# Kernel tuning notes

Measured on AMD Instinct MI355X. Metric: run time of the kernel, lower is better.

## Reference

```python
import jax, jax.numpy as jnp
import numpy as np

B, T, D, K = 64, 1024, 256, 1024
DECAY = 0.99      # ema_decay
BETA = 0.25       # commitment_cost
EPS = 1e-5


def setup_inputs() -> dict:
    key = jax.random.key(0)
    k1, k2 = jax.random.split(key, 2)
    z = jax.random.normal(k1, (B, T, D), dtype=jnp.float32)
    # nn.init.uniform_(embedding.weight, -1/K, 1/K)
    embed = jax.random.uniform(k2, (K, D), dtype=jnp.float32,
                               minval=-1.0 / K, maxval=1.0 / K)
    ema_count = jnp.zeros((K,), dtype=jnp.float32)
    ema_weight = embed  # buffer initialized as a clone of the weight
    return {"z": z, "embed": embed, "ema_count": ema_count, "ema_weight": ema_weight}


def reference(z, embed, ema_count, ema_weight):
    Bq, Tq, Dq = z.shape
    zf = z.reshape(-1, Dq)  # [N, D], N = B*T
    # squared euclidean distances: [N, K]
    dist = (zf * zf).sum(axis=1, keepdims=True) \
        - 2.0 * (zf @ embed.T) \
        + (embed * embed).sum(axis=1)
    idx = jnp.argmin(dist, axis=1)                      # [N]
    q = embed[idx].reshape(Bq, Tq, Dq)                  # nearest codebook vectors

    commit = jnp.mean((z - jax.lax.stop_gradient(q)) ** 2)
    codebook = jnp.mean((q - jax.lax.stop_gradient(z)) ** 2)
    vq_loss = codebook + BETA * commit

    # straight-through estimator
    q_st = z + jax.lax.stop_gradient(q - z)

    # EMA codebook update (training-mode, no_grad in torch)
    counts = jax.ops.segment_sum(jnp.ones((zf.shape[0],), zf.dtype), idx, num_segments=K)
    dw = jax.ops.segment_sum(zf, idx, num_segments=K)   # one_hot.T @ z_flat, [K, D]
    new_count = DECAY * ema_count + (1.0 - DECAY) * counts
    new_ema_w = DECAY * ema_weight + (1.0 - DECAY) * dw
    n = new_count.sum()
    cs = (new_count + EPS) / (n + K * EPS) * n          # laplace-smoothed counts
    new_embed = new_ema_w / cs[:, None]

    return (q_st, vq_loss, idx.reshape(Bq, Tq), new_embed, new_count, new_ema_w)
```

## Files before the change

### kernel.cpp

```cpp
#include <hip/hip_runtime.h>
#include <cfloat>

#define N_Q     65536
#define D_DIM   256
#define K_CODES 1024
#define DELTA   0.004f
#define MARGIN  0.001f
#define SW_CAP  1536

#define OUT_QST   0
#define OUT_LOSS  16777216
#define OUT_IDX   16777217
#define OUT_EMBED 16842753
#define OUT_COUNT 17104897
#define OUT_EMAW  17105921

#define WS_IDX    0u
#define WS_ZZ     262144u
#define WS_PERM   524288u
#define WS_PACK   786432u
#define WS_EN     1310720u
#define WS_ICNT   1314816u
#define WS_OFFS   1318912u
#define WS_OFFW   1323008u
#define WS_CNTF   1327104u
#define WS_CS     1331200u
#define WS_ET     1335296u
#define WS_LOSSB  1859584u

typedef short          bf16x8 __attribute__((ext_vector_type(8)));
typedef unsigned short u16x8  __attribute__((ext_vector_type(8)));
typedef float          f32x4  __attribute__((ext_vector_type(4)));

__device__ inline unsigned short f2bf(float x) {
    unsigned u = __float_as_uint(x);
    u += 0x7FFFu + ((u >> 16) & 1u);
    return (unsigned short)(u >> 16);
}
__device__ inline float bf2f(unsigned short h) {
    return __uint_as_float((unsigned)h << 16);
}
__device__ inline u16x8 pack8(float4 a, float4 b) {
    u16x8 p;
    p[0]=f2bf(a.x); p[1]=f2bf(a.y); p[2]=f2bf(a.z); p[3]=f2bf(a.w);
    p[4]=f2bf(b.x); p[5]=f2bf(b.y); p[6]=f2bf(b.z); p[7]=f2bf(b.w);
    return p;
}
__device__ inline void gll16(const void* g, void* l) {
    __builtin_amdgcn_global_load_lds(
        (const __attribute__((address_space(1))) unsigned int*)g,
        (__attribute__((address_space(3))) unsigned int*)l, 16, 0, 0);
}

__global__ void rownorm2_kernel(const float* __restrict__ x, float* __restrict__ out)
{
    int wave = threadIdx.x >> 6, lane = threadIdx.x & 63;
    int row  = blockIdx.x * 4 + wave;
    const float4 v = *(const float4*)&x[(size_t)row * D_DIM + lane * 4];
    float s = v.x * v.x + v.y * v.y + v.z * v.z + v.w * v.w;
    #pragma unroll
    for (int m = 32; m >= 1; m >>= 1) s += __shfl_down(s, m, 64);
    if (lane == 0) out[row] = s;
}

__global__ void conv_e_kernel(const float* __restrict__ e,
                              unsigned short* __restrict__ et)
{
    int tid = blockIdx.x * 256 + threadIdx.x;
    int k16 = tid >> 9, d8 = (tid >> 4) & 31, col = tid & 15;
    const float* src = &e[(size_t)(k16 * 16 + col) * D_DIM + d8 * 8];
    float4 a = *(const float4*)&src[0];
    float4 b = *(const float4*)&src[4];
    *(u16x8*)&et[(size_t)tid * 8] = pack8(a, b);
}

__launch_bounds__(256, 2)
__global__ void sweep_kernel(const float* __restrict__ z,
                             const float* __restrict__ embed,
                             const unsigned short* __restrict__ et,
                             const float* __restrict__ enorm,
                             const float* __restrict__ zz,
                             unsigned long long* __restrict__ pack)
{
    __shared__ unsigned short Eb[2][16384];
    __shared__ unsigned list[SW_CAP];
    __shared__ unsigned short s1h[SW_CAP];
    __shared__ float Ens[K_CODES];
    __shared__ float rminS[128];
    __shared__ int lcnt;

    const int t = threadIdx.x;
    const int w = t >> 6, lane = t & 63;
    const int col = lane & 15, quad = lane >> 4;
    const int qbase = blockIdx.x * 128;

    if (t == 0) lcnt = 0;
    for (int i = t; i < K_CODES; i += 256) Ens[i] = enorm[i];

    {
        const unsigned short* src = et + w * 4096 + lane * 8;
        unsigned short* dst = &Eb[0][w * 4096];
        #pragma unroll
        for (int i = 0; i < 8; ++i) gll16(src + i * 512, dst + i * 512);
    }

    bf16x8 A[2][8];
    #pragma unroll
    for (int rt = 0; rt < 2; ++rt)
        #pragma unroll
        for (int ds = 0; ds < 8; ++ds) {
            const float* zp = &z[(size_t)(qbase + w*32 + rt*16 + col) * D_DIM
                                 + ds*32 + quad*8];
            float4 a = *(const float4*)zp;
            float4 b = *(const float4*)(zp + 4);
            u16x8 p = pack8(a, b);
            A[rt][ds] = *(bf16x8*)&p;
        }

    float rmin[2][4];
    #pragma unroll
    for (int rt = 0; rt < 2; ++rt)
        #pragma unroll
        for (int rg = 0; rg < 4; ++rg)
            rmin[rt][rg] = FLT_MAX;

    __syncthreads();

    #pragma unroll 1
    for (int kc = 0; kc < 16; ++kc) {
        if (kc < 15) {
            const unsigned short* src = et + (kc + 1) * 16384 + w * 4096 + lane * 8;
            unsigned short* dst = &Eb[(kc + 1) & 1][w * 4096];
            #pragma unroll
            for (int i = 0; i < 8; ++i) gll16(src + i * 512, dst + i * 512);
        }

        const unsigned short* buf = Eb[kc & 1];
        f32x4 acc[2][4];
        #pragma unroll
        for (int rt = 0; rt < 2; ++rt)
            #pragma unroll
            for (int ct = 0; ct < 4; ++ct)
                acc[rt][ct] = (f32x4){0.f, 0.f, 0.f, 0.f};

        #pragma unroll
        for (int ds = 0; ds < 8; ++ds) {
            bf16x8 B[4];
            #pragma unroll
            for (int ct = 0; ct < 4; ++ct)
                B[ct] = *(const bf16x8*)&buf[((ct*32 + ds*4 + quad)*16 + col)*8];
            #pragma unroll
            for (int ct = 0; ct < 4; ++ct) {
                acc[0][ct] = __builtin_amdgcn_mfma_f32_16x16x32_bf16(A[0][ds], B[ct], acc[0][ct], 0, 0, 0);
                acc[1][ct] = __builtin_amdgcn_mfma_f32_16x16x32_bf16(A[1][ds], B[ct], acc[1][ct], 0, 0, 0);
            }
        }

        float en[4];
        #pragma unroll
        for (int ct = 0; ct < 4; ++ct) en[ct] = Ens[kc*64 + ct*16 + col];

        #pragma unroll
        for (int rt = 0; rt < 2; ++rt) {
            #pragma unroll
            for (int rg = 0; rg < 4; ++rg) {
                float s1v[4];
                #pragma unroll
                for (int ct = 0; ct < 4; ++ct)
                    s1v[ct] = fmaf(-2.0f, acc[rt][ct][rg], en[ct]);
                float m = fminf(fminf(s1v[0], s1v[1]), fminf(s1v[2], s1v[3]));
                #pragma unroll
                for (int mm = 1; mm < 16; mm <<= 1)
                    m = fminf(m, __shfl_xor(m, mm, 64));
                rmin[rt][rg] = fminf(rmin[rt][rg], m);
                float thr = rmin[rt][rg] + DELTA;
                #pragma unroll
                for (int ct = 0; ct < 4; ++ct) {
                    if (s1v[ct] <= thr) {
                        int k    = kc*64 + ct*16 + col;
                        int qloc = w*32 + rt*16 + quad*4 + rg;
                        int pos  = atomicAdd(&lcnt, 1);
                        if (pos < SW_CAP) {
                            list[pos] = ((unsigned)qloc << 10) | (unsigned)k;
                            s1h[pos]  = f2bf(s1v[ct]);
                        } else {
                            int qg = qbase + qloc;
                            double dd = 0.0;
                            for (int d = 0; d < D_DIM; d += 4) {
                                float4 a = *(const float4*)&z[(size_t)qg*D_DIM + d];
                                float4 b = *(const float4*)&embed[(size_t)k*D_DIM + d];
                                dd += (double)a.x*b.x + (double)a.y*b.y
                                    + (double)a.z*b.z + (double)a.w*b.w;
                            }
                            float s = (zz[qg] - 2.0f*(float)dd) + en[ct];
                            unsigned long long pk =
                                ((unsigned long long)__float_as_uint(s) << 32) | (unsigned)k;
                            atomicMin(&pack[qg], pk);
                        }
                    }
                }
            }
        }

        __syncthreads();
    }

    if (col == 0) {
        #pragma unroll
        for (int rt = 0; rt < 2; ++rt)
            #pragma unroll
            for (int rg = 0; rg < 4; ++rg)
                rminS[w*32 + rt*16 + quad*4 + rg] = rmin[rt][rg];
    }
    __syncthreads();

    int cnt = min(lcnt, SW_CAP);
    int gid = t >> 3, gl = t & 7;
    for (int e = gid; e < cnt; e += 32) {
        unsigned ent = list[e];
        int qloc = (int)(ent >> 10), k = (int)(ent & 1023u);
        if (bf2f(s1h[e]) > rminS[qloc] + (DELTA + MARGIN)) continue;
        int qg = qbase + qloc;
        const float* zp  = &z[(size_t)qg * D_DIM + gl * 32];
        const float* epf = &embed[(size_t)k * D_DIM + gl * 32];
        double d0 = 0.0, d1 = 0.0;
        #pragma unroll
        for (int i = 0; i < 4; ++i) {
            float4 a  = *(const float4*)&zp[i*8];
            float4 b  = *(const float4*)&epf[i*8];
            float4 c  = *(const float4*)&zp[i*8 + 4];
            float4 dv = *(const float4*)&epf[i*8 + 4];
            d0 += (double)a.x*b.x + (double)a.y*b.y + (double)a.z*b.z + (double)a.w*b.w;
            d1 += (double)c.x*dv.x + (double)c.y*dv.y + (double)c.z*dv.z + (double)c.w*dv.w;
        }
        double dd = d0 + d1;
        #pragma unroll
        for (int m = 1; m < 8; m <<= 1) dd += __shfl_xor(dd, m, 64);
        if (gl == 0) {
            float s = (zz[qg] - 2.0f*(float)dd) + enorm[k];
            unsigned long long pk =
                ((unsigned long long)__float_as_uint(s) << 32) | (unsigned)k;
            atomicMin(&pack[qg], pk);
        }
    }
}

__global__ void unpack_kernel(const unsigned long long* __restrict__ pack,
                              int* __restrict__ idx_i,
                              float* __restrict__ idx_f,
                              int* __restrict__ icnt)
{
    int n = blockIdx.x * 256 + threadIdx.x;
    int k = (int)(pack[n] & 0xffffffffull);
    idx_i[n] = k;
    idx_f[n] = (float)k;
    atomicAdd(&icnt[k], 1);
}

__global__ void scan_kernel(const int* __restrict__ icnt,
                            int* __restrict__ offs,
                            int* __restrict__ offw,
                            float* __restrict__ cntf)
{
    __shared__ int s[1024];
    int t = threadIdx.x;
    int v0 = icnt[t];
    s[t] = v0;
    __syncthreads();
    for (int d = 1; d < 1024; d <<= 1) {
        int v = (t >= d) ? s[t - d] : 0;
        __syncthreads();
        s[t] += v;
        __syncthreads();
    }
    int excl = s[t] - v0;
    offs[t] = excl;
    offw[t] = excl;
    cntf[t] = (float)v0;
}

__global__ void fill_kernel(const int* __restrict__ idx,
                            int* __restrict__ offw,
                            int* __restrict__ perm)
{
    int n = blockIdx.x * 256 + threadIdx.x;
    int k = idx[n];
    int pos = atomicAdd(&offw[k], 1);
    perm[pos] = n;
}

__global__ void qst_loss_kernel(const float* __restrict__ z,
                                const float* __restrict__ embed,
                                const int* __restrict__ idx,
                                float* __restrict__ qst,
                                double* __restrict__ lossb)
{
    int tid = blockIdx.x * blockDim.x + threadIdx.x;
    int e0  = tid * 4;
    int n   = e0 >> 8, d = e0 & 255;
    int k   = idx[n];
    const float4 q4 = *(const float4*)&embed[(size_t)k * D_DIM + d];
    const float4 z4 = *(const float4*)&z[e0];
    float4 o;
    o.x = z4.x + (q4.x - z4.x);
    o.y = z4.y + (q4.y - z4.y);
    o.z = z4.z + (q4.z - z4.z);
    o.w = z4.w + (q4.w - z4.w);
    *(float4*)&qst[e0] = o;
    float dx = z4.x - q4.x, dy = z4.y - q4.y, dz = z4.z - q4.z, dw = z4.w - q4.w;
    float s = dx * dx + dy * dy + dz * dz + dw * dw;
    #pragma unroll
    for (int m = 32; m >= 1; m >>= 1) s += __shfl_down(s, m, 64);
    __shared__ float ps[4];
    int wave = threadIdx.x >> 6, lane = threadIdx.x & 63;
    if (lane == 0) ps[wave] = s;
    __syncthreads();
    if (threadIdx.x == 0)
        atomicAdd(&lossb[blockIdx.x & 1023],
                  (double)((ps[0] + ps[1]) + (ps[2] + ps[3])));
}

__global__ void fin_counts_kernel(const float* __restrict__ ema_count,
                                  const float* __restrict__ cntf,
                                  const double* __restrict__ lossb,
                                  float* __restrict__ out_count,
                                  float* __restrict__ out_loss,
                                  float* __restrict__ cs)
{
    __shared__ float  red[1024];
    __shared__ double dred[1024];
    int t = threadIdx.x;
    float c = 0.99f * ema_count[t] + 0.01f * cntf[t];
    out_count[t] = c;
    red[t]  = c;
    dred[t] = lossb[t];
    __syncthreads();
    for (int s = 512; s >= 1; s >>= 1) {
        if (t < s) { red[t] += red[t + s]; dred[t] += dred[t + s]; }
        __syncthreads();
    }
    float n = red[0];
    cs[t] = (c + 1e-5f) / (n + 1024.0f * 1e-5f) * n;
    if (t == 0) {
        float m = (float)(dred[0] / (double)((size_t)N_Q * D_DIM));
        out_loss[0] = m + 0.25f * m;
    }
}

__global__ void accum_embed_kernel(const float* __restrict__ z,
                                   const int* __restrict__ perm,
                                   const int* __restrict__ icnt,
                                   const int* __restrict__ offs,
                                   const float* __restrict__ cs,
                                   const float* __restrict__ ema_w,
                                   float* __restrict__ out_embed,
                                   float* __restrict__ out_emaw)
{
    __shared__ int rows[256];
    int k = blockIdx.x, t = threadIdx.x;
    int cnt = icnt[k], off = offs[k];
    double a0 = 0.0, a1 = 0.0, a2 = 0.0, a3 = 0.0;
    for (int base = 0; base < cnt; base += 256) {
        int m = min(256, cnt - base);
        __syncthreads();
        if (t < m) rows[t] = perm[off + base + t];
        __syncthreads();
        int r = 0;
        for (; r + 4 <= m; r += 4) {
            a0 += (double)z[(size_t)rows[r+0] * D_DIM + t];
            a1 += (double)z[(size_t)rows[r+1] * D_DIM + t];
            a2 += (double)z[(size_t)rows[r+2] * D_DIM + t];
            a3 += (double)z[(size_t)rows[r+3] * D_DIM + t];
        }
        for (; r < m; ++r) a0 += (double)z[(size_t)rows[r] * D_DIM + t];
    }
    double acc = (a0 + a1) + (a2 + a3);
    float w = 0.99f * ema_w[(size_t)k * D_DIM + t] + 0.01f * (float)acc;
    out_emaw[(size_t)k * D_DIM + t]  = w;
    out_embed[(size_t)k * D_DIM + t] = w / cs[k];
}

extern "C" void kernel_launch(void* const* d_in, const int* in_sizes, int n_in,
                              void* d_out, int out_size, void* d_ws, size_t ws_size,
                              hipStream_t stream)
{
    const float* z          = (const float*)d_in[0];
    const float* embed      = (const float*)d_in[1];
    const float* ema_count  = (const float*)d_in[2];
    const float* ema_weight = (const float*)d_in[3];
    float* out = (float*)d_out;
    char*  ws  = (char*)d_ws;

    int*      ws_idx  = (int*)(ws + WS_IDX);
    float*    ws_zz   = (float*)(ws + WS_ZZ);
    int*      ws_perm = (int*)(ws + WS_PERM);
    unsigned long long* ws_pack = (unsigned long long*)(ws + WS_PACK);
    float*    ws_en   = (float*)(ws + WS_EN);
    int*      ws_icnt = (int*)(ws + WS_ICNT);
    int*      ws_offs = (int*)(ws + WS_OFFS);
    int*      ws_offw = (int*)(ws + WS_OFFW);
    float*    ws_cntf = (float*)(ws + WS_CNTF);
    float*    ws_cs   = (float*)(ws + WS_CS);
    unsigned short* ws_et = (unsigned short*)(ws + WS_ET);
    double*   ws_lb   = (double*)(ws + WS_LOSSB);

    hipMemsetAsync(ws + WS_PACK,  0xFF, (size_t)N_Q * 8, stream);
    hipMemsetAsync(ws + WS_ICNT,  0, 4096, stream);
    hipMemsetAsync(ws + WS_LOSSB, 0, 8192, stream);

    rownorm2_kernel<<<K_CODES / 4, 256, 0, stream>>>(embed, ws_en);
    rownorm2_kernel<<<N_Q / 4,     256, 0, stream>>>(z, ws_zz);
    conv_e_kernel<<<128, 256, 0, stream>>>(embed, ws_et);

    sweep_kernel<<<N_Q / 128, 256, 0, stream>>>(z, embed, ws_et, ws_en, ws_zz,
                                                ws_pack);

    unpack_kernel<<<N_Q / 256, 256, 0, stream>>>(ws_pack, ws_idx,
                                                 out + OUT_IDX, ws_icnt);
    scan_kernel<<<1, 1024, 0, stream>>>(ws_icnt, ws_offs, ws_offw, ws_cntf);
    fill_kernel<<<N_Q / 256, 256, 0, stream>>>(ws_idx, ws_offw, ws_perm);
    qst_loss_kernel<<<(N_Q * (D_DIM / 4)) / 256, 256, 0, stream>>>(
        z, embed, ws_idx, out + OUT_QST, ws_lb);
    fin_counts_kernel<<<1, 1024, 0, stream>>>(ema_count, ws_cntf, ws_lb,
                                              out + OUT_COUNT, out + OUT_LOSS, ws_cs);
    accum_embed_kernel<<<K_CODES, 256, 0, stream>>>(z, ws_perm, ws_icnt, ws_offs,
                                                    ws_cs, ema_weight,
                                                    out + OUT_EMBED, out + OUT_EMAW);
}
```

Baseline: 332.2 us.

## Fuse prep kernels, compute z norms in sweep, defer overflow rescoring to spill kernel

Replaces the three memsets, the two rownorm launches and the embed conversion with a single prep kernel. The z row norms are now computed inside the sweep kernel from the values it already loads for the bf16 conversion. Candidate overflow past the shared list no longer runs a serial fp64 dot product inline; entries go to a global spill list that a separate kernel rescores. The per-row min reduction is batched across eight rows using ds_swizzle instead of shfl_xor. This trades fewer launches and less z traffic for an extra spill launch, and the spill buffer reuses the idx workspace region.

```diff
diff --git a/kernel.cpp b/kernel.cpp
--- a/kernel.cpp
+++ b/kernel.cpp
@@ -7,6 +7,7 @@
 #define DELTA   0.004f
 #define MARGIN  0.001f
 #define SW_CAP  1536
+#define SPILL_CAP 65536
 
 #define OUT_QST   0
 #define OUT_LOSS  16777216
@@ -27,6 +28,7 @@
 #define WS_CS     1331200u
 #define WS_ET     1335296u
 #define WS_LOSSB  1859584u
+#define WS_SPCNT  1867776u
 
 typedef short          bf16x8 __attribute__((ext_vector_type(8)));
 typedef unsigned short u16x8  __attribute__((ext_vector_type(8)));
@@ -51,27 +53,48 @@
         (const __attribute__((address_space(1))) unsigned int*)g,
         (__attribute__((address_space(3))) unsigned int*)l, 16, 0, 0);
 }
-
-__global__ void rownorm2_kernel(const float* __restrict__ x, float* __restrict__ out)
-{
-    int wave = threadIdx.x >> 6, lane = threadIdx.x & 63;
-    int row  = blockIdx.x * 4 + wave;
-    const float4 v = *(const float4*)&x[(size_t)row * D_DIM + lane * 4];
-    float s = v.x * v.x + v.y * v.y + v.z * v.z + v.w * v.w;
-    #pragma unroll
-    for (int m = 32; m >= 1; m >>= 1) s += __shfl_down(s, m, 64);
-    if (lane == 0) out[row] = s;
-}
-
-__global__ void conv_e_kernel(const float* __restrict__ e,
-                              unsigned short* __restrict__ et)
-{
-    int tid = blockIdx.x * 256 + threadIdx.x;
-    int k16 = tid >> 9, d8 = (tid >> 4) & 31, col = tid & 15;
-    const float* src = &e[(size_t)(k16 * 16 + col) * D_DIM + d8 * 8];
-    float4 a = *(const float4*)&src[0];
-    float4 b = *(const float4*)&src[4];
-    *(u16x8*)&et[(size_t)tid * 8] = pack8(a, b);
+#define SWZMIN(x, PAT) fminf((x), __int_as_float( \
+    __builtin_amdgcn_ds_swizzle(__float_as_int(x), (PAT))))
+
+__global__ void prep_kernel(const float* __restrict__ embed,
+                            unsigned short* __restrict__ et,
+                            unsigned long long* __restrict__ pack,
+                            float* __restrict__ enorm,
+                            int* __restrict__ icnt,
+                            double* __restrict__ lossb,
+                            int* __restrict__ spc)
+{
+    int b = blockIdx.x, t = threadIdx.x;
+    if (b < 128) {
+        int tid = b * 256 + t;
+        int k16 = tid >> 9, d8 = (tid >> 4) & 31, col = tid & 15;
+        const float* src = &embed[(size_t)(k16 * 16 + col) * D_DIM + d8 * 8];
+        float4 a = *(const float4*)&src[0];
+        float4 c = *(const float4*)&src[4];
+        *(u16x8*)&et[(size_t)tid * 8] = pack8(a, c);
+        unsigned long long* p = pack + (size_t)tid * 2;
+        p[0] = ~0ull; p[1] = ~0ull;
+    } else {
+        int b2 = b - 128;
+        int wave = t >> 6, lane = t & 63;
+        int rbase = (b2 * 4 + wave) * 8;
+        for (int i = 0; i < 8; ++i) {
+            int r = rbase + i;
+            const float4 v = *(const float4*)&embed[(size_t)r * D_DIM + lane * 4];
+            float s = v.x * v.x + v.y * v.y + v.z * v.z + v.w * v.w;
+            #pragma unroll
+            for (int m = 32; m >= 1; m >>= 1) s += __shfl_down(s, m, 64);
+            if (lane == 0) enorm[r] = s;
+        }
+        if (b2 == 0) {
+            #pragma unroll
+            for (int i = 0; i < 4; ++i) {
+                icnt[t * 4 + i] = 0;
+                lossb[t * 4 + i] = 0.0;
+            }
+            if (t == 0) *spc = 0;
+        }
+    }
 }
 
 __launch_bounds__(256, 2)
@@ -79,14 +102,17 @@
                              const float* __restrict__ embed,
                              const unsigned short* __restrict__ et,
                              const float* __restrict__ enorm,
-                             const float* __restrict__ zz,
-                             unsigned long long* __restrict__ pack)
+                             float* __restrict__ zzg,
+                             unsigned long long* __restrict__ pack,
+                             unsigned* __restrict__ spill,
+                             int* __restrict__ spc)
 {
     __shared__ unsigned short Eb[2][16384];
     __shared__ unsigned list[SW_CAP];
     __shared__ unsigned short s1h[SW_CAP];
     __shared__ float Ens[K_CODES];
     __shared__ float rminS[128];
+    __shared__ float zzS[128];
     __shared__ int lcnt;
 
     const int t = threadIdx.x;
@@ -106,23 +132,30 @@
 
     bf16x8 A[2][8];
     #pragma unroll
-    for (int rt = 0; rt < 2; ++rt)
+    for (int rt = 0; rt < 2; ++rt) {
+        float s = 0.f;
         #pragma unroll
         for (int ds = 0; ds < 8; ++ds) {
             const float* zp = &z[(size_t)(qbase + w*32 + rt*16 + col) * D_DIM
                                  + ds*32 + quad*8];
             float4 a = *(const float4*)zp;
             float4 b = *(const float4*)(zp + 4);
+            s += a.x*a.x + a.y*a.y + a.z*a.z + a.w*a.w
+               + b.x*b.x + b.y*b.y + b.z*b.z + b.w*b.w;
             u16x8 p = pack8(a, b);
             A[rt][ds] = *(bf16x8*)&p;
         }
-
-    float rmin[2][4];
+        s += __shfl_xor(s, 16, 64);
+        s += __shfl_xor(s, 32, 64);
+        if (quad == 0) {
+            zzg[qbase + w*32 + rt*16 + col] = s;
+            zzS[w*32 + rt*16 + col] = s;
+        }
+    }
+
+    float rmin[8];
     #pragma unroll
-    for (int rt = 0; rt < 2; ++rt)
-        #pragma unroll
-        for (int rg = 0; rg < 4; ++rg)
-            rmin[rt][rg] = FLT_MAX;
+    for (int i = 0; i < 8; ++i) rmin[i] = FLT_MAX;
 
     __syncthreads();
 
@@ -156,51 +189,66 @@
             }
         }
 
-        float en[4];
-        #pragma unroll
-        for (int ct = 0; ct < 4; ++ct) en[ct] = Ens[kc*64 + ct*16 + col];
-
-        #pragma unroll
-        for (int rt = 0; rt < 2; ++rt) {
+        float en4[4];
+        #pragma unroll
+        for (int ct = 0; ct < 4; ++ct) en4[ct] = Ens[kc*64 + ct*16 + col];
+
+        float s1v[2][4][4];
+        #pragma unroll
+        for (int rt = 0; rt < 2; ++rt)
+            #pragma unroll
+            for (int ct = 0; ct < 4; ++ct)
+                #pragma unroll
+                for (int rg = 0; rg < 4; ++rg)
+                    s1v[rt][ct][rg] = fmaf(-2.0f, acc[rt][ct][rg], en4[ct]);
+
+        float m8[8];
+        #pragma unroll
+        for (int rt = 0; rt < 2; ++rt)
+            #pragma unroll
+            for (int rg = 0; rg < 4; ++rg)
+                m8[rt*4+rg] = fminf(fminf(s1v[rt][0][rg], s1v[rt][1][rg]),
+                                    fminf(s1v[rt][2][rg], s1v[rt][3][rg]));
+
+        #pragma unroll
+        for (int i = 0; i < 8; ++i) m8[i] = SWZMIN(m8[i], 0x041F);
+        #pragma unroll
+        for (int i = 0; i < 8; ++i) m8[i] = SWZMIN(m8[i], 0x081F);
+        #pragma unroll
+        for (int i = 0; i < 8; ++i) m8[i] = SWZMIN(m8[i], 0x101F);
+        #pragma unroll
+        for (int i = 0; i < 8; ++i) m8[i] = SWZMIN(m8[i], 0x201F);
+
+        float thrv[8];
+        #pragma unroll
+        for (int i = 0; i < 8; ++i) {
+            rmin[i] = fminf(rmin[i], m8[i]);
+            thrv[i] = rmin[i] + DELTA;
+        }
+
+        #pragma unroll
+        for (int rt = 0; rt < 2; ++rt)
             #pragma unroll
             for (int rg = 0; rg < 4; ++rg) {
-                float s1v[4];
-                #pragma unroll
-                for (int ct = 0; ct < 4; ++ct)
-                    s1v[ct] = fmaf(-2.0f, acc[rt][ct][rg], en[ct]);
-                float m = fminf(fminf(s1v[0], s1v[1]), fminf(s1v[2], s1v[3]));
-                #pragma unroll
-                for (int mm = 1; mm < 16; mm <<= 1)
-                    m = fminf(m, __shfl_xor(m, mm, 64));
-                rmin[rt][rg] = fminf(rmin[rt][rg], m);
-                float thr = rmin[rt][rg] + DELTA;
+                float th = thrv[rt*4+rg];
                 #pragma unroll
                 for (int ct = 0; ct < 4; ++ct) {
-                    if (s1v[ct] <= thr) {
+                    if (s1v[rt][ct][rg] <= th) {
                         int k    = kc*64 + ct*16 + col;
                         int qloc = w*32 + rt*16 + quad*4 + rg;
                         int pos  = atomicAdd(&lcnt, 1);
                         if (pos < SW_CAP) {
                             list[pos] = ((unsigned)qloc << 10) | (unsigned)k;
-                            s1h[pos]  = f2bf(s1v[ct]);
+                            s1h[pos]  = f2bf(s1v[rt][ct][rg]);
                         } else {
-                            int qg = qbase + qloc;
-                            double dd = 0.0;
-                            for (int d = 0; d < D_DIM; d += 4) {
-                                float4 a = *(const float4*)&z[(size_t)qg*D_DIM + d];
-                                float4 b = *(const float4*)&embed[(size_t)k*D_DIM + d];
-                                dd += (double)a.x*b.x + (double)a.y*b.y
-                                    + (double)a.z*b.z + (double)a.w*b.w;
-                            }
-                            float s = (zz[qg] - 2.0f*(float)dd) + en[ct];
-                            unsigned long long pk =
-                                ((unsigned long long)__float_as_uint(s) << 32) | (unsigned)k;
-                            atomicMin(&pack[qg], pk);
+                            int sp = atomicAdd(spc, 1);
+                            if (sp < SPILL_CAP)
+                                spill[sp] = ((unsigned)(qbase + qloc) << 10)
+                                          | (unsigned)k;
                         }
                     }
                 }
             }
-        }
 
         __syncthreads();
     }
@@ -210,7 +258,7 @@
         for (int rt = 0; rt < 2; ++rt)
             #pragma unroll
             for (int rg = 0; rg < 4; ++rg)
-                rminS[w*32 + rt*16 + quad*4 + rg] = rmin[rt][rg];
+                rminS[w*32 + rt*16 + quad*4 + rg] = rmin[rt*4+rg];
     }
     __syncthreads();
 
@@ -234,6 +282,41 @@
             d1 += (double)c.x*dv.x + (double)c.y*dv.y + (double)c.z*dv.z + (double)c.w*dv.w;
         }
         double dd = d0 + d1;
+        #pragma unroll
+        for (int m = 1; m < 8; m <<= 1) dd += __shfl_xor(dd, m, 64);
+        if (gl == 0) {
+            float s = (zzS[qloc] - 2.0f*(float)dd) + Ens[k];
+            unsigned long long pk =
+                ((unsigned long long)__float_as_uint(s) << 32) | (unsigned)k;
+            atomicMin(&pack[qg], pk);
+        }
+    }
+}
+
+__global__ void spill_kernel(const float* __restrict__ z,
+                             const float* __restrict__ embed,
+                             const float* __restrict__ enorm,
+                             const float* __restrict__ zz,
+                             const unsigned* __restrict__ spill,
+                             const int* __restrict__ spc,
+                             unsigned long long* __restrict__ pack)
+{
+    int cnt = *spc; if (cnt > SPILL_CAP) cnt = SPILL_CAP;
+    int gid = (blockIdx.x * 256 + threadIdx.x) >> 3, gl = threadIdx.x & 7;
+    int stride = (gridDim.x * 256) >> 3;
+    for (int e = gid; e < cnt; e += stride) {
+        unsigned ent = spill[e];
+        int qg = (int)(ent >> 10), k = (int)(ent & 1023u);
+        const float* zp  = &z[(size_t)qg * D_DIM + gl * 32];
+        const float* epf = &embed[(size_t)k * D_DIM + gl * 32];
+        double dd = 0.0;
+        #pragma unroll
+        for (int i = 0; i < 8; ++i) {
+            float4 a = *(const float4*)&zp[i*4];
+            float4 b = *(const float4*)&epf[i*4];
+            dd += (double)a.x*b.x + (double)a.y*b.y
+                + (double)a.z*b.z + (double)a.w*b.w;
+        }
         #pragma unroll
         for (int m = 1; m < 8; m <<= 1) dd += __shfl_xor(dd, m, 64);
         if (gl == 0) {
@@ -392,6 +475,7 @@
     char*  ws  = (char*)d_ws;
 
     int*      ws_idx  = (int*)(ws + WS_IDX);
+    unsigned* ws_spill= (unsigned*)(ws + WS_IDX);
     float*    ws_zz   = (float*)(ws + WS_ZZ);
     int*      ws_perm = (int*)(ws + WS_PERM);
     unsigned long long* ws_pack = (unsigned long long*)(ws + WS_PACK);
@@ -403,17 +487,16 @@
     float*    ws_cs   = (float*)(ws + WS_CS);
     unsigned short* ws_et = (unsigned short*)(ws + WS_ET);
     double*   ws_lb   = (double*)(ws + WS_LOSSB);
-
-    hipMemsetAsync(ws + WS_PACK,  0xFF, (size_t)N_Q * 8, stream);
-    hipMemsetAsync(ws + WS_ICNT,  0, 4096, stream);
-    hipMemsetAsync(ws + WS_LOSSB, 0, 8192, stream);
-
-    rownorm2_kernel<<<K_CODES / 4, 256, 0, stream>>>(embed, ws_en);
-    rownorm2_kernel<<<N_Q / 4,     256, 0, stream>>>(z, ws_zz);
-    conv_e_kernel<<<128, 256, 0, stream>>>(embed, ws_et);
+    int*      ws_spc  = (int*)(ws + WS_SPCNT);
+
+    prep_kernel<<<160, 256, 0, stream>>>(embed, ws_et, ws_pack, ws_en,
+                                         ws_icnt, ws_lb, ws_spc);
 
     sweep_kernel<<<N_Q / 128, 256, 0, stream>>>(z, embed, ws_et, ws_en, ws_zz,
-                                                ws_pack);
+                                                ws_pack, ws_spill, ws_spc);
+
+    spill_kernel<<<32, 256, 0, stream>>>(z, embed, ws_en, ws_zz,
+                                         ws_spill, ws_spc, ws_pack);
 
     unpack_kernel<<<N_Q / 256, 256, 0, stream>>>(ws_pack, ws_idx,
                                                  out + OUT_IDX, ws_icnt);
```

New measurement: 298.4 us. 10.2% less time.
